# Optimization experiments

Measured on AMD Instinct MI355X. Metric: run time of the kernel, lower is better.

Reference implementation:

```python
import jax, jax.numpy as jnp
import numpy as np

WORD_VOCAB = 100000
TAG_VOCAB = 50
WD = 300
TD = 100
EMB = WD + TD          # 400: LSTM input size AND hidden size
H = EMB
L = 512


def setup_inputs() -> dict:
    key = jax.random.key(0)
    ks = jax.random.split(key, 16)
    def p(k, shape):
        return jax.random.normal(k, shape, dtype=jnp.float32) * 0.05
    return {
        "words_idx_tensor": jax.random.randint(ks[0], (1, L), 0, WORD_VOCAB),
        "tags_idx_tensor": jax.random.randint(ks[1], (1, L), 0, TAG_VOCAB),
        "max_length": L,
        "word_emb": p(ks[2], (WORD_VOCAB, WD)),
        "tag_emb": p(ks[3], (TAG_VOCAB, TD)),
        # stacked [fwd, bwd] directions per layer (PyTorch LSTM gate order i,f,g,o)
        "w_ih_l0": p(ks[4], (2, 4 * H, EMB)),
        "w_hh_l0": p(ks[5], (2, 4 * H, H)),
        "b_ih_l0": p(ks[6], (2, 4 * H)),
        "b_hh_l0": p(ks[7], (2, 4 * H)),
        "w_ih_l1": p(ks[8], (2, 4 * H, 2 * H)),
        "w_hh_l1": p(ks[9], (2, 4 * H, H)),
        "b_ih_l1": p(ks[10], (2, 4 * H)),
        "b_hh_l1": p(ks[11], (2, 4 * H)),
        "fc1_w": p(ks[12], (1, 4 * H)),
        "fc1_b": p(ks[13], (1,)),
    }


def _lstm_dir(x, w_ih, w_hh, b_ih, b_hh, reverse):
    # x: [T, in]. Precompute input projections once (hoisted out of scan).
    xi = x @ w_ih.T + b_ih + b_hh  # [T, 4H]
    Hn = w_hh.shape[1]

    def step(carry, g_in):
        h, c = carry
        g = g_in + h @ w_hh.T
        i, f, gg, o = jnp.split(g, 4, axis=-1)
        c = jax.nn.sigmoid(f) * c + jax.nn.sigmoid(i) * jnp.tanh(gg)
        h = jax.nn.sigmoid(o) * jnp.tanh(c)
        return (h, c), h

    init = (jnp.zeros((Hn,), x.dtype), jnp.zeros((Hn,), x.dtype))
    _, hs = jax.lax.scan(step, init, xi, reverse=reverse)
    return hs  # [T, H]


def _bilstm(x, w_ih, w_hh, b_ih, b_hh):
    fwd = _lstm_dir(x, w_ih[0], w_hh[0], b_ih[0], b_hh[0], False)
    bwd = _lstm_dir(x, w_ih[1], w_hh[1], b_ih[1], b_hh[1], True)
    return jnp.concatenate([fwd, bwd], axis=-1)  # [T, 2H]


def reference(words_idx_tensor, tags_idx_tensor, max_length, word_emb, tag_emb,
              w_ih_l0, w_hh_l0, b_ih_l0, b_hh_l0,
              w_ih_l1, w_hh_l1, b_ih_l1, b_hh_l1,
              fc1_w, fc1_b):
    # Embedding lookup + concat; batch dim of size 1 squeezed (torch's
    # view(shape[1], shape[0], -1) yields [L, 1, emb] for the LSTM).
    x = jnp.concatenate([word_emb[words_idx_tensor[0]],
                         tag_emb[tags_idx_tensor[0]]], axis=-1)  # [L, EMB]

    h = _bilstm(x, w_ih_l0, w_hh_l0, b_ih_l0, b_hh_l0)   # [L, 2H]
    h = _bilstm(h, w_ih_l1, w_hh_l1, b_ih_l1, b_hh_l1)   # [L, 2H]

    # Pairwise edge scores: tanh(W @ [h_i; h_j] + b).
    # Split W into head/dep halves -> two small GEMMs + broadcast outer-sum,
    # avoiding the O(L^2 * 4H) concatenated feature tensor.
    two_h = fc1_w.shape[1] // 2
    s = h @ fc1_w[:, :two_h].T   # [L, 1]
    t = h @ fc1_w[:, two_h:].T   # [L, 1]
    scores = jnp.tanh(s[:, None, :] + t[None, :, :] + fc1_b)  # [L, L, 1]
    # torch stacks (i outer, j inner) -> [L*L, 1, 1]
    return scores.reshape(max_length * max_length, 1, 1)
```

## Files before the change

### kernel.cpp

```cpp
#include <hip/hip_runtime.h>

#define SEQ 512
#define HID 400
#define GATES 1600
#define E1 800
#define TEAM 10
#define RECGRID 160

__device__ __forceinline__ float bf2f(unsigned short u) {
    return __uint_as_float(((unsigned)u) << 16);
}
__device__ __forceinline__ unsigned short f2bf(float f) {
    unsigned u = __float_as_uint(f);
    u += 0x7FFFu + ((u >> 16) & 1u);
    return (unsigned short)(u >> 16);
}
__device__ __forceinline__ float sigm(float x) { return 1.f / (1.f + __expf(-x)); }
__device__ __forceinline__ float tanh_f(float x) {
    float xc = fminf(fmaxf(x, -15.f), 15.f);
    float e = __expf(2.f * xc);
    return (e - 1.f) / (e + 1.f);
}
__device__ __forceinline__ float loadx(const void* p, size_t i, int isbf) {
    return isbf ? bf2f(((const unsigned short*)p)[i]) : ((const float*)p)[i];
}

__global__ void detect_kernel(const unsigned short* __restrict__ wemb,
                              unsigned* __restrict__ dtf) {
    __shared__ int cnt;
    if (threadIdx.x == 0) cnt = 0;
    __syncthreads();
    int pass = 0;
    for (int i = 0; i < 8; ++i) {
        unsigned short u = wemb[threadIdx.x * 8 + i];
        int e = (u >> 7) & 0xFF;
        pass += (e >= 100 && e <= 130) ? 1 : 0;
    }
    atomicAdd(&cnt, pass);
    __syncthreads();
    if (threadIdx.x == 0) *dtf = (cnt >= 1843) ? 1u : 0u;
}

__global__ void embed_kernel(const int* __restrict__ words, const int* __restrict__ tags,
                             const void* __restrict__ wemb, const void* __restrict__ temb,
                             float* __restrict__ x ,
                             const unsigned* __restrict__ dtf) {
    int t = blockIdx.x;
    int w = words[t], g = tags[t];
    int isbf = (int)*dtf;
    for (int k = threadIdx.x; k < HID; k += blockDim.x) {
        float v = (k < 300) ? loadx(wemb, (size_t)w * 300 + k, isbf)
                            : loadx(temb, (size_t)g * 100 + (k - 300), isbf);
        x[(size_t)t * HID + k] = v;
    }
}

__global__ __launch_bounds__(256) void proj_kernel(
        const void* __restrict__ Araw, int tagged,
        const void* __restrict__ Wraw ,
        const void* __restrict__ bihRaw, const void* __restrict__ bhhRaw,
        float* __restrict__ xi ,
        int K, const unsigned* __restrict__ dtf) {
    const int isbf = (int)*dtf;
    __shared__ float As[16][132];
    __shared__ float Ws[16][68];
    int tid = threadIdx.x;
    int t0 = blockIdx.x * 128, n0 = blockIdx.y * 64, dir = blockIdx.z;
    int arow = tid >> 1, akoff = (tid & 1) * 8;
    int wrow = tid >> 2, wkoff = (tid & 3) * 4;
    int tx = (tid & 15) * 4;
    int ty = (tid >> 4) * 8;

    const float* Af = (const float*)Araw + (size_t)(t0 + arow) * K + akoff;
    const unsigned long long* At = (const unsigned long long*)Araw +
                                   (size_t)(t0 + arow) * K + akoff;
    size_t wbase = (size_t)(dir * GATES + n0 + wrow) * K + wkoff;
    const float* Wf = (const float*)Wraw + wbase;
    const unsigned short* Wh = (const unsigned short*)Wraw + wbase;

    float acc[8][4] = {};
    for (int k0 = 0; k0 < K; k0 += 16) {
        float av8[8];
        if (tagged) {
            ulonglong2 q0 = *(const ulonglong2*)(At + k0);
            ulonglong2 q1 = *(const ulonglong2*)(At + k0 + 2);
            ulonglong2 q2 = *(const ulonglong2*)(At + k0 + 4);
            ulonglong2 q3 = *(const ulonglong2*)(At + k0 + 6);
            av8[0] = __uint_as_float((unsigned)q0.x); av8[1] = __uint_as_float((unsigned)q0.y);
            av8[2] = __uint_as_float((unsigned)q1.x); av8[3] = __uint_as_float((unsigned)q1.y);
            av8[4] = __uint_as_float((unsigned)q2.x); av8[5] = __uint_as_float((unsigned)q2.y);
            av8[6] = __uint_as_float((unsigned)q3.x); av8[7] = __uint_as_float((unsigned)q3.y);
        } else {
            float4 a0 = *(const float4*)(Af + k0);
            float4 a1 = *(const float4*)(Af + k0 + 4);
            av8[0] = a0.x; av8[1] = a0.y; av8[2] = a0.z; av8[3] = a0.w;
            av8[4] = a1.x; av8[5] = a1.y; av8[6] = a1.z; av8[7] = a1.w;
        }
        float4 wv;
        if (isbf) {
            ushort4 w4 = *(const ushort4*)(Wh + k0);
            wv = make_float4(bf2f(w4.x), bf2f(w4.y), bf2f(w4.z), bf2f(w4.w));
        } else {
            wv = *(const float4*)(Wf + k0);
        }
        __syncthreads();
#pragma unroll
        for (int i = 0; i < 8; ++i) As[akoff + i][arow] = av8[i];
        Ws[wkoff + 0][wrow] = wv.x; Ws[wkoff + 1][wrow] = wv.y;
        Ws[wkoff + 2][wrow] = wv.z; Ws[wkoff + 3][wrow] = wv.w;
        __syncthreads();
#pragma unroll
        for (int kk = 0; kk < 16; ++kk) {
            float4 alo = *(const float4*)&As[kk][ty];
            float4 ahi = *(const float4*)&As[kk][ty + 4];
            float4 w4  = *(const float4*)&Ws[kk][tx];
            float av[8] = {alo.x, alo.y, alo.z, alo.w, ahi.x, ahi.y, ahi.z, ahi.w};
            float wvv[4] = {w4.x, w4.y, w4.z, w4.w};
#pragma unroll
            for (int i = 0; i < 8; ++i)
#pragma unroll
                for (int j = 0; j < 4; ++j)
                    acc[i][j] = fmaf(av[i], wvv[j], acc[i][j]);
        }
    }
    float bias[4];
#pragma unroll
    for (int j = 0; j < 4; ++j) {
        int n = n0 + tx + j;
        bias[j] = loadx(bihRaw, dir * GATES + n, isbf) + loadx(bhhRaw, dir * GATES + n, isbf);
    }
    float* xout = xi + (size_t)dir * SEQ * GATES;
#pragma unroll
    for (int i = 0; i < 8; ++i) {
        int t = t0 + ty + i;
        float4 o = make_float4(acc[i][0] + bias[0], acc[i][1] + bias[1],
                               acc[i][2] + bias[2], acc[i][3] + bias[3]);
        *(float4*)&xout[(size_t)t * GATES + n0 + tx] = o;
    }
}

struct SyncArea { unsigned cnt[8]; unsigned claim[2]; unsigned pad[6]; };

__global__ __launch_bounds__(512, 2) void rec_kernel(
        const float* __restrict__ xi ,
        const void* __restrict__ whhRaw ,
        unsigned long long* __restrict__ hx  ,
        unsigned long long* __restrict__ hx2 ,
        unsigned tagbase, SyncArea* __restrict__ sy,
        const unsigned* __restrict__ dtf) {
    int tid = threadIdx.x;
    __shared__ int role[2];
    if (tid == 0) {
        unsigned xcd = __builtin_amdgcn_s_getreg((3 << 11) | 20) & 0xFu;
        unsigned rank = atomicAdd(&sy->cnt[xcd], 1u);
        unsigned group = rank / TEAM;
        unsigned key = 1u + xcd * 64u + group;
        if ((rank % TEAM) == TEAM - 1) {
            unsigned prev = atomicCAS(&sy->claim[0], 0u, key);
            if (prev != 0u) atomicCAS(&sy->claim[1], 0u, key);
        }
        int dir = -1;
        while (dir < 0) {
            unsigned c0 = __hip_atomic_load(&sy->claim[0], __ATOMIC_RELAXED,
                                            __HIP_MEMORY_SCOPE_AGENT);
            unsigned c1 = __hip_atomic_load(&sy->claim[1], __ATOMIC_RELAXED,
                                            __HIP_MEMORY_SCOPE_AGENT);
            if (c0 == key) dir = 0;
            else if (c1 == key) dir = 1;
            else if (c0 != 0u && c1 != 0u) dir = 2;
        }
        role[0] = dir;
        role[1] = (int)(rank % TEAM);
    }
    __syncthreads();
    const int dir = role[0];
    const int wg  = role[1];
    if (dir == 2) return;

    int chunk = tid & 15;
    int rg    = tid >> 4;
    const int isbf = (int)*dtf;
    const int dirHID = dir * HID;

    __shared__ __align__(16) float hbuf[HID];
    __shared__ __align__(16) float partials[160][20];
    __shared__ __align__(16) float gates[160];

    float wv[5][25];
#pragma unroll
    for (int r = 0; r < 5; ++r) {
        int lr = rg * 5 + r;
        int jj = lr >> 2, gg = lr & 3;
        int grow = gg * HID + wg * 40 + jj;
        size_t base = ((size_t)dir * GATES + grow) * HID + chunk * 25;
        if (isbf) {
            const unsigned short* p = (const unsigned short*)whhRaw + base;
#pragma unroll
            for (int c = 0; c < 25; ++c) wv[r][c] = bf2f(p[c]);
        } else {
            const float* p = (const float*)whhRaw + base;
#pragma unroll
            for (int c = 0; c < 25; ++c) wv[r][c] = p[c];
        }
    }

    int xrow = 0;
    if (tid < 160) { int jj = tid >> 2, gg = tid & 3; xrow = gg * HID + wg * 40 + jj; }
    const float* xibase = xi + (size_t)dir * SEQ * GATES;
    float cstate = 0.f;
    size_t myelem = dirHID + wg * 40 + tid;

#pragma unroll 1
    for (int k = 0; k < SEQ; ++k) {
        int t = dir ? (SEQ - 1 - k) : k;
        float xiv = 0.f;
        if (tid < 160) xiv = xibase[(size_t)t * GATES + xrow];

        if (k > 0) {
            int tprev = dir ? (t + 1) : (t - 1);
            if (tid < HID) {
                const unsigned want = tagbase + (unsigned)k;
                size_t eidx = (size_t)tprev * E1 + dirHID + tid;
                const volatile unsigned long long* p =
                    (const volatile unsigned long long*)&hx[eidx];
                unsigned long long w;
                int spin = 0;
                for (;;) {
                    w = *p;
                    if ((unsigned)(w >> 32) == want) break;
                    if (++spin >= 24) {
                        w = __hip_atomic_load(&hx2[eidx], __ATOMIC_RELAXED,
                                              __HIP_MEMORY_SCOPE_AGENT);
                        if ((unsigned)(w >> 32) == want) break;
                        spin = 0;
                    }
                }
                hbuf[tid] = __uint_as_float((unsigned)w);
            }
        } else {
            if (tid < HID) hbuf[tid] = 0.f;
        }
        __syncthreads();

        float acc[5] = {0.f, 0.f, 0.f, 0.f, 0.f};
#pragma unroll
        for (int c = 0; c < 25; ++c) {
            float hv = hbuf[chunk * 25 + c];
#pragma unroll
            for (int r = 0; r < 5; ++r)
                acc[r] = fmaf(wv[r][c], hv, acc[r]);
        }
#pragma unroll
        for (int r = 0; r < 5; ++r) partials[rg * 5 + r][chunk] = acc[r];
        __syncthreads();

        if (tid < 160) {
            const float4* pr = (const float4*)&partials[tid][0];
            float4 p0 = pr[0], p1 = pr[1], p2 = pr[2], p3 = pr[3];
            float s = p0.x + p0.y + p0.z + p0.w
                    + p1.x + p1.y + p1.z + p1.w
                    + p2.x + p2.y + p2.z + p2.w
                    + p3.x + p3.y + p3.z + p3.w;
            gates[tid] = s + xiv;
        }
        __syncthreads();

        if (tid < 40) {
            float4 g4 = *(const float4*)&gates[tid * 4];
            float ig = sigm(g4.x), fg = sigm(g4.y), cg = tanh_f(g4.z), og = sigm(g4.w);
            cstate = fg * cstate + ig * cg;
            float hv = og * tanh_f(cstate);
            unsigned long long w =
                ((unsigned long long)(tagbase + (unsigned)k + 1u) << 32) |
                (unsigned long long)(unsigned)__float_as_uint(hv);
            size_t eidx = (size_t)t * E1 + myelem;
            *(volatile unsigned long long*)&hx[eidx] = w;
            __hip_atomic_store(&hx2[eidx], w, __ATOMIC_RELAXED,
                               __HIP_MEMORY_SCOPE_AGENT);
        }
    }
}

__global__ void st_kernel(const unsigned long long* __restrict__ h1x ,
                          const void* __restrict__ fw ,
                          float* __restrict__ sv, float* __restrict__ tv,
                          const unsigned* __restrict__ dtf) {
    int i = blockIdx.x;
    int lane = threadIdx.x;
    int isbf = (int)*dtf;
    float s = 0.f, t = 0.f;
    for (int j = lane; j < E1; j += 64) {
        float hv = __uint_as_float((unsigned)h1x[(size_t)i * E1 + j]);
        s += hv * loadx(fw, j, isbf);
        t += hv * loadx(fw, E1 + j, isbf);
    }
#pragma unroll
    for (int o = 32; o > 0; o >>= 1) {
        s += __shfl_xor(s, o, 64);
        t += __shfl_xor(t, o, 64);
    }
    if (lane == 0) { sv[i] = s; tv[i] = t; }
}

__global__ void scores_kernel(const float* __restrict__ sv, const float* __restrict__ tv,
                              const void* __restrict__ fb, void* __restrict__ out,
                              const unsigned* __restrict__ dtf) {
    int idx = blockIdx.x * blockDim.x + threadIdx.x;
    int i = idx >> 9, j = idx & 511;
    int isbf = (int)*dtf;
    float v = tanh_f(sv[i] + tv[j] + loadx(fb, 0, isbf));
    if (isbf) ((unsigned short*)out)[idx] = f2bf(v);
    else      ((float*)out)[idx] = v;
}

static constexpr size_t OFF_X    = 0;
static constexpr size_t OFF_XI   = 819200;
static constexpr size_t OFF_SV   = 7372800;
static constexpr size_t OFF_TV   = 7374848;
static constexpr size_t OFF_DTF  = 7376896;
static constexpr size_t OFF_SYNC = 7376960;
static constexpr size_t OFF_HX   = 7377216;
static constexpr size_t OFF_HX2  = 10654016;

extern "C" void kernel_launch(void* const* d_in, const int* in_sizes, int n_in,
                              void* d_out, int out_size, void* d_ws, size_t ws_size,
                              hipStream_t stream) {
    const int* words = (const int*)d_in[0];
    const int* tags  = (const int*)d_in[1];
    const void* wemb = d_in[3];
    const void* temb = d_in[4];
    const void* wih0 = d_in[5];
    const void* whh0 = d_in[6];
    const void* bih0 = d_in[7];
    const void* bhh0 = d_in[8];
    const void* wih1 = d_in[9];
    const void* whh1 = d_in[10];
    const void* bih1 = d_in[11];
    const void* bhh1 = d_in[12];
    const void* fw   = d_in[13];
    const void* fb   = d_in[14];

    char* ws = (char*)d_ws;
    float* x               = (float*)(ws + OFF_X);
    float* xi              = (float*)(ws + OFF_XI);
    float* sv              = (float*)(ws + OFF_SV);
    float* tv              = (float*)(ws + OFF_TV);
    unsigned* dtf          = (unsigned*)(ws + OFF_DTF);
    SyncArea* sync0        = (SyncArea*)(ws + OFF_SYNC);
    SyncArea* sync1        = (SyncArea*)(ws + OFF_SYNC + 64);
    unsigned long long* hx  = (unsigned long long*)(ws + OFF_HX);
    unsigned long long* hx2 = (unsigned long long*)(ws + OFF_HX2);

    hipMemsetAsync(ws + OFF_SYNC, 0, 128, stream);
    detect_kernel<<<1, 256, 0, stream>>>((const unsigned short*)wemb, dtf);
    embed_kernel<<<SEQ, 128, 0, stream>>>(words, tags, wemb, temb, x, dtf);

    proj_kernel<<<dim3(4, 25, 2), 256, 0, stream>>>(x, 0, wih0, bih0, bhh0, xi, HID, dtf);
    rec_kernel<<<RECGRID, 512, 0, stream>>>(xi, whh0, hx, hx2, 0u, sync0, dtf);

    proj_kernel<<<dim3(4, 25, 2), 256, 0, stream>>>(hx, 1, wih1, bih1, bhh1, xi, E1, dtf);
    rec_kernel<<<RECGRID, 512, 0, stream>>>(xi, whh1, hx, hx2, 512u, sync1, dtf);

    st_kernel<<<SEQ, 64, 0, stream>>>(hx, fw, sv, tv, dtf);
    scores_kernel<<<(SEQ * SEQ) / 256, 256, 0, stream>>>(sv, tv, fb, d_out, dtf);
}
```

Baseline: 1.947 ms.

## Spread LSTM recurrence across 25 workgroups per direction with vectorized h loads

Each recurrent workgroup now handles 16 hidden units (64 gate rows) instead of 40, so 25 workgroups per direction cooperate and the grid grows to 256. Per-thread register weights shrink from 5x25 to 2x25, which cuts per-step FMA latency. The hidden vector is stored in shared memory with a padded stride of 28 so each thread reads its 25-element chunk with float4 loads. In exchange, more workgroups must poll and exchange the hidden state every step, which raises global synchronization traffic and requires all 50 teams to be co-resident.

```diff
diff --git a/kernel.cpp b/kernel.cpp
--- a/kernel.cpp
+++ b/kernel.cpp
@@ -4,8 +4,10 @@
 #define HID 400
 #define GATES 1600
 #define E1 800
-#define TEAM 10
-#define RECGRID 160
+#define TEAM 25
+#define RECGRID 256
+#define ROWS 64
+#define HSL 16
 
 __device__ __forceinline__ float bf2f(unsigned short u) {
     return __uint_as_float(((unsigned)u) << 16);
@@ -177,21 +179,21 @@
     const int wg  = role[1];
     if (dir == 2) return;
 
-    int chunk = tid & 15;
-    int rg    = tid >> 4;
-    const int isbf = (int)*dtf;
+    const int chunk = tid & 15;
+    const int rg    = tid >> 4;
+    const int isbf  = (int)*dtf;
     const int dirHID = dir * HID;
 
-    __shared__ __align__(16) float hbuf[HID];
-    __shared__ __align__(16) float partials[160][20];
-    __shared__ __align__(16) float gates[160];
-
-    float wv[5][25];
-#pragma unroll
-    for (int r = 0; r < 5; ++r) {
-        int lr = rg * 5 + r;
+    __shared__ __align__(16) float hbuf[16 * 28];
+    __shared__ __align__(16) float partials[ROWS][20];
+    __shared__ __align__(16) float gates[ROWS];
+
+    float wv[2][25];
+#pragma unroll
+    for (int r = 0; r < 2; ++r) {
+        int lr = rg * 2 + r;
         int jj = lr >> 2, gg = lr & 3;
-        int grow = gg * HID + wg * 40 + jj;
+        int grow = gg * HID + wg * HSL + jj;
         size_t base = ((size_t)dir * GATES + grow) * HID + chunk * 25;
         if (isbf) {
             const unsigned short* p = (const unsigned short*)whhRaw + base;
@@ -205,16 +207,17 @@
     }
 
     int xrow = 0;
-    if (tid < 160) { int jj = tid >> 2, gg = tid & 3; xrow = gg * HID + wg * 40 + jj; }
+    if (tid < ROWS) { int jj = tid >> 2, gg = tid & 3; xrow = gg * HID + wg * HSL + jj; }
+    const int hIdx = (tid / 25) * 28 + (tid % 25);
     const float* xibase = xi + (size_t)dir * SEQ * GATES;
     float cstate = 0.f;
-    size_t myelem = dirHID + wg * 40 + tid;
+    size_t myelem = dirHID + wg * HSL + tid;
 
 #pragma unroll 1
     for (int k = 0; k < SEQ; ++k) {
         int t = dir ? (SEQ - 1 - k) : k;
         float xiv = 0.f;
-        if (tid < 160) xiv = xibase[(size_t)t * GATES + xrow];
+        if (tid < ROWS) xiv = xibase[(size_t)t * GATES + xrow];
 
         if (k > 0) {
             int tprev = dir ? (t + 1) : (t - 1);
@@ -235,26 +238,35 @@
                         spin = 0;
                     }
                 }
-                hbuf[tid] = __uint_as_float((unsigned)w);
+                hbuf[hIdx] = __uint_as_float((unsigned)w);
             }
         } else {
-            if (tid < HID) hbuf[tid] = 0.f;
-        }
-        __syncthreads();
-
-        float acc[5] = {0.f, 0.f, 0.f, 0.f, 0.f};
+            if (tid < HID) hbuf[hIdx] = 0.f;
+        }
+        __syncthreads();
+
+        const float* hb = &hbuf[chunk * 28];
+        float4 h4a = *(const float4*)(hb + 0);
+        float4 h4b = *(const float4*)(hb + 4);
+        float4 h4c = *(const float4*)(hb + 8);
+        float4 h4d = *(const float4*)(hb + 12);
+        float4 h4e = *(const float4*)(hb + 16);
+        float4 h4f = *(const float4*)(hb + 20);
+        float hv[25] = {h4a.x, h4a.y, h4a.z, h4a.w, h4b.x, h4b.y, h4b.z, h4b.w,
+                        h4c.x, h4c.y, h4c.z, h4c.w, h4d.x, h4d.y, h4d.z, h4d.w,
+                        h4e.x, h4e.y, h4e.z, h4e.w, h4f.x, h4f.y, h4f.z, h4f.w,
+                        hb[24]};
+        float acc0 = 0.f, acc1 = 0.f;
 #pragma unroll
         for (int c = 0; c < 25; ++c) {
-            float hv = hbuf[chunk * 25 + c];
-#pragma unroll
-            for (int r = 0; r < 5; ++r)
-                acc[r] = fmaf(wv[r][c], hv, acc[r]);
-        }
-#pragma unroll
-        for (int r = 0; r < 5; ++r) partials[rg * 5 + r][chunk] = acc[r];
-        __syncthreads();
-
-        if (tid < 160) {
+            acc0 = fmaf(wv[0][c], hv[c], acc0);
+            acc1 = fmaf(wv[1][c], hv[c], acc1);
+        }
+        partials[rg * 2 + 0][chunk] = acc0;
+        partials[rg * 2 + 1][chunk] = acc1;
+        __syncthreads();
+
+        if (tid < ROWS) {
             const float4* pr = (const float4*)&partials[tid][0];
             float4 p0 = pr[0], p1 = pr[1], p2 = pr[2], p3 = pr[3];
             float s = p0.x + p0.y + p0.z + p0.w
@@ -265,14 +277,14 @@
         }
         __syncthreads();
 
-        if (tid < 40) {
+        if (tid < HSL) {
             float4 g4 = *(const float4*)&gates[tid * 4];
             float ig = sigm(g4.x), fg = sigm(g4.y), cg = tanh_f(g4.z), og = sigm(g4.w);
             cstate = fg * cstate + ig * cg;
-            float hv = og * tanh_f(cstate);
+            float hv2 = og * tanh_f(cstate);
             unsigned long long w =
                 ((unsigned long long)(tagbase + (unsigned)k + 1u) << 32) |
-                (unsigned long long)(unsigned)__float_as_uint(hv);
+                (unsigned long long)(unsigned)__float_as_uint(hv2);
             size_t eidx = (size_t)t * E1 + myelem;
             *(volatile unsigned long long*)&hx[eidx] = w;
             __hip_atomic_store(&hx2[eidx], w, __ATOMIC_RELAXED,
```

Result: faster. 1.791 ms (-8.0%).
